# Kernel tuning notes

Measured on AMD Instinct MI355X. Metric: run time of the kernel, lower is better.

The kernel has to match this reference:

```python
import jax, jax.numpy as jnp
import numpy as np

B, D, H = 2048, 1024, 16
DH = D // H            # 64 head dim
R = DH // 2            # 32 random-feature dim (kernel_type has no 'northogonal')
EPS = 1e-3             # keras LayerNormalization default epsilon


def _orthogonal(seed):
    # mirrors random_orthogonal(shape=(1,H,1,DH,R)): QR of flat (H*DH, R) matrix
    rng = np.random.default_rng(seed)
    a = rng.standard_normal((H * DH, R)).astype(np.float32)
    q, r = np.linalg.qr(a)
    q = q * np.sign(np.diag(r))[None, :]
    return jnp.asarray(q.reshape(H, DH, R))


def setup_inputs() -> dict:
    key = jax.random.key(0)
    ks = jax.random.split(key, 8)
    inp = {
        "x": jax.random.normal(ks[0], (B, D), jnp.float32),
        # states start as small positive values so den = phi4(q) . new_z > 0
        "s": jax.random.uniform(ks[1], (B, D * R), jnp.float32),
        "z": jax.random.uniform(ks[2], (B, R * H), jnp.float32),
        "ln1_g": jnp.ones((D,), jnp.float32),
        "ln1_b": jnp.zeros((D,), jnp.float32),
        "ln2_g": jnp.ones((D,), jnp.float32),
        "ln2_b": jnp.zeros((D,), jnp.float32),
        "W_attn": jax.random.normal(ks[3], (D, 3 * D), jnp.float32) * 0.02,
        "b_attn": jnp.zeros((3 * D,), jnp.float32),
        "W_proj": jax.random.normal(ks[4], (D, D), jnp.float32) * 0.02,
        "b_proj": jnp.zeros((D,), jnp.float32),
        "W_fc": jax.random.normal(ks[5], (D, 4 * D), jnp.float32) * 0.02,
        "b_fc": jnp.zeros((4 * D,), jnp.float32),
        "W_mp": jax.random.normal(ks[6], (4 * D, D), jnp.float32) * 0.02,
        "b_mp": jnp.zeros((D,), jnp.float32),
    }
    for i in range(4):
        inp[f"w{i + 1}"] = _orthogonal(100 + i)
    return inp


def _ln(x, g, b):
    m = jnp.mean(x, axis=-1, keepdims=True)
    v = jnp.var(x, axis=-1, keepdims=True)
    return g * (x - m) * jax.lax.rsqrt(v + EPS) + b


def _phi(x, w):
    # x: [B,H,dh], w: [H,dh,R] orthogonal random features; kernel 'sigmoid'
    return jax.nn.sigmoid(jnp.einsum('bhd,hdr->bhr', x, w))


def reference(x, s, z, ln1_g, ln1_b, ln2_g, ln2_b, W_attn, b_attn,
              W_proj, b_proj, W_fc, b_fc, W_mp, b_mp, w1, w2, w3, w4):
    bsz = x.shape[0]
    h1 = _ln(x, ln1_g, ln1_b)
    qkv = h1 @ W_attn + b_attn                      # [B, 3D]
    q, k, v = jnp.split(qkv, 3, axis=1)
    q = q.reshape(bsz, H, DH)
    k = k.reshape(bsz, H, DH)
    v = v.reshape(bsz, H, DH)
    s4 = s.reshape(bsz, H, R, DH)
    z3 = z.reshape(bsz, H, R)
    # kernelized linear-attention state update (outer-product accumulation)
    new_s = s4 + jnp.einsum('bhr,bhd->bhrd', _phi(k, w1), v)   # [B,H,R,DH]
    new_z = z3 + _phi(k, w2)                                   # [B,H,R]
    num = jnp.einsum('bhr,bhrd->bhd', _phi(q, w3), new_s)      # [B,H,DH]
    den = jnp.einsum('bhr,bhr->bh', _phi(q, w4), new_z)[..., None]
    head = (num / den).reshape(bsz, D)
    attention = head @ W_proj + b_proj
    h2 = _ln(attention + x, ln2_g, ln2_b)          # dropout: inference mode
    ffn = jax.nn.gelu(h2 @ W_fc + b_fc, approximate=False) @ W_mp + b_mp
    out = h2 + ffn
    return out, new_s.reshape(bsz, D * R), new_z.reshape(bsz, R * H)
```

## Files before the change

### kernel.cpp

```cpp
#include <hip/hip_runtime.h>
#include <hip/hip_bf16.h>
#include <math.h>


#define Bsz 2048
#define Dm  1024
#define Hh  16
#define DHd 64
#define Rr  32

typedef __bf16 bf16x8 __attribute__((ext_vector_type(8)));
typedef float  f32x4  __attribute__((ext_vector_type(4)));

__device__ __forceinline__ __bf16 f2bf(float x) { return (__bf16)x; }

#define GLOAD_LDS16(g, l) __builtin_amdgcn_global_load_lds(               \
    (const __attribute__((address_space(1))) void*)(g),                   \
    (__attribute__((address_space(3))) void*)(l), 16, 0, 0)

__global__ __launch_bounds__(256) void wtrans_kernel(
    const float* __restrict__ W, __bf16* __restrict__ Wt, int K, int N)
{
  __shared__ float tile[32][33];
  const int tx = threadIdx.x & 31;
  const int ty0 = threadIdx.x >> 5;
  const int bn = blockIdx.x * 32;
  const int bk = blockIdx.y * 32;
#pragma unroll
  for (int j = 0; j < 4; ++j)
    tile[ty0 + j * 8][tx] = W[(size_t)(bk + ty0 + j * 8) * N + bn + tx];
  __syncthreads();
#pragma unroll
  for (int j = 0; j < 4; ++j) {
    const int ny = ty0 + j * 8;
    Wt[(size_t)(bn + ny) * K + bk + tx] = f2bf(tile[tx][ny]);
  }
}

template<bool ADD, typename TA>
__global__ __launch_bounds__(256) void ln_kernel(
    const TA* __restrict__ a, const float* __restrict__ b2,
    const float* __restrict__ g, const float* __restrict__ beta,
    __bf16* __restrict__ outb, float* __restrict__ outf)
{
  const int row = blockIdx.x;
  const int t = threadIdx.x;
  const size_t base = (size_t)row * Dm;
  float vals[4];
#pragma unroll
  for (int i = 0; i < 4; ++i) {
    const int c = t * 4 + i;
    float v = (float)a[base + c];
    if (ADD) v += b2[base + c];
    vals[i] = v;
  }
  float sm = 0.f, sq = 0.f;
#pragma unroll
  for (int i = 0; i < 4; ++i) { sm += vals[i]; sq += vals[i] * vals[i]; }
  for (int off = 32; off > 0; off >>= 1) {
    sm += __shfl_down(sm, off);
    sq += __shfl_down(sq, off);
  }
  __shared__ float smw[4], sqw[4];
  if ((t & 63) == 0) { smw[t >> 6] = sm; sqw[t >> 6] = sq; }
  __syncthreads();
  const float S  = smw[0] + smw[1] + smw[2] + smw[3];
  const float SS = sqw[0] + sqw[1] + sqw[2] + sqw[3];
  const float mean = S * (1.f / Dm);
  const float var  = SS * (1.f / Dm) - mean * mean;
  const float inv  = rsqrtf(var + 1e-3f);
#pragma unroll
  for (int i = 0; i < 4; ++i) {
    const int c = t * 4 + i;
    const float r = g[c] * ((vals[i] - mean) * inv) + beta[c];
    outb[base + c] = f2bf(r);
    if (ADD) outf[base + c] = r;
  }
}

template<int BM, int BN, bool GELU, bool RES, bool OUTF32>
__global__ __launch_bounds__(256) void gemm_kernel(
    const __bf16* __restrict__ A, const __bf16* __restrict__ Bt,
    const float* __restrict__ bias, const float* __restrict__ res,
    void* __restrict__ Cv, int M, int N, int K)
{
  constexpr int FM = BM / 32;
  constexpr int FN = BN / 32;
  __shared__ __align__(16) __bf16 lsA[BM * 32];
  __shared__ __align__(16) __bf16 lsB[BN * 32];
  const int t = threadIdx.x;
  const int wave = t >> 6, lane = t & 63;
  const int quad = lane >> 4, l16 = lane & 15;
  const int wm = wave >> 1, wn = wave & 1;
  const int bm = blockIdx.x * BM, bn = blockIdx.y * BN;

  const int srow = lane >> 2, scol = (lane & 3) * 8;
  const __bf16* Ag  = A  + (size_t)(bm + wave * 16 + srow) * K + scol;
  const __bf16* Bg0 = Bt + (size_t)(bn + wave * (BN / 4) + srow) * K + scol;
  const __bf16* Bg1 = Bt + (size_t)(bn + wave * (BN / 4) + 16 + srow) * K + scol;
  __bf16* lA  = &lsA[wave * 16 * 32];
  __bf16* lB0 = &lsB[wave * (BN / 4) * 32];
  __bf16* lB1 = &lsB[(wave * (BN / 4) + 16) * 32];

  f32x4 acc[FM][FN];
#pragma unroll
  for (int mi = 0; mi < FM; ++mi)
#pragma unroll
    for (int ni = 0; ni < FN; ++ni)
      acc[mi][ni] = (f32x4){0.f, 0.f, 0.f, 0.f};

  for (int kt = 0; kt < K; kt += 32) {
    GLOAD_LDS16(Ag + kt, lA);
    GLOAD_LDS16(Bg0 + kt, lB0);
    if constexpr (BN == 128) GLOAD_LDS16(Bg1 + kt, lB1);
    __syncthreads();
    bf16x8 af[FM], bfr[FN];
#pragma unroll
    for (int mi = 0; mi < FM; ++mi)
      af[mi] = *(const bf16x8*)&lsA[(wm * (BM / 2) + mi * 16 + l16) * 32 + quad * 8];
#pragma unroll
    for (int ni = 0; ni < FN; ++ni)
      bfr[ni] = *(const bf16x8*)&lsB[(wn * (BN / 2) + ni * 16 + l16) * 32 + quad * 8];
#pragma unroll
    for (int mi = 0; mi < FM; ++mi)
#pragma unroll
      for (int ni = 0; ni < FN; ++ni)
        acc[mi][ni] = __builtin_amdgcn_mfma_f32_16x16x32_bf16(
            af[mi], bfr[ni], acc[mi][ni], 0, 0, 0);
    __syncthreads();
  }

#pragma unroll
  for (int mi = 0; mi < FM; ++mi) {
    const int row0 = bm + wm * (BM / 2) + mi * 16 + quad * 4;
#pragma unroll
    for (int ni = 0; ni < FN; ++ni) {
      const int col = bn + wn * (BN / 2) + ni * 16 + l16;
      const float bv = bias[col];
#pragma unroll
      for (int i = 0; i < 4; ++i) {
        const int row = row0 + i;
        float v = acc[mi][ni][i] + bv;
        if (GELU) v = 0.5f * v * (1.0f + erff(v * 0.70710678118654752f));
        if (RES) v += res[(size_t)row * N + col];
        if (OUTF32) ((float*)Cv)[(size_t)row * N + col] = v;
        else        ((__bf16*)Cv)[(size_t)row * N + col] = f2bf(v);
      }
    }
  }
}

__global__ __launch_bounds__(64) void attn_kernel(
    const float* __restrict__ qkv, const float* __restrict__ s,
    const float* __restrict__ z,
    const float* __restrict__ w1, const float* __restrict__ w2,
    const float* __restrict__ w3, const float* __restrict__ w4,
    float* __restrict__ new_s, float* __restrict__ new_z,
    __bf16* __restrict__ head)
{
  const int bh = blockIdx.x;
  const int b = bh >> 4, h = bh & 15;
  const int tid = threadIdx.x;
  __shared__ float ksh[64], qsh[64];
  __shared__ float phish[4][32];
  __shared__ float nzsh[32];

  const float* qrow = qkv + (size_t)b * (3 * Dm);
  const float qv = qrow[h * 64 + tid];
  const float kv = qrow[Dm + h * 64 + tid];
  const float vv = qrow[2 * Dm + h * 64 + tid];
  qsh[tid] = qv; ksh[tid] = kv;
  __syncthreads();

  {
    const int r = tid & 31;
    const float* wm[4] = {w1, w2, w3, w4};
    for (int mm = (tid >> 5); mm < 4; mm += 2) {
      const float* w = wm[mm] + (size_t)h * (DHd * Rr) + r;
      const float* src = (mm < 2) ? ksh : qsh;
      float acc = 0.f;
#pragma unroll 8
      for (int d = 0; d < 64; ++d) acc += src[d] * w[(size_t)d * 32];
      phish[mm][r] = 1.f / (1.f + expf(-acc));
    }
  }
  __syncthreads();

  const size_t zbase = (size_t)b * (Rr * Hh) + h * Rr;
  if (tid < 32) {
    const float nz = z[zbase + tid] + phish[1][tid];
    new_z[zbase + tid] = nz;
    nzsh[tid] = nz;
  }
  __syncthreads();

  float den = 0.f;
#pragma unroll
  for (int r = 0; r < 32; ++r) den += phish[3][r] * nzsh[r];

  const size_t sbase = ((size_t)b * Hh + h) * (Rr * DHd);
  float num = 0.f;
#pragma unroll 4
  for (int r = 0; r < 32; ++r) {
    const float ns = s[sbase + r * 64 + tid] + phish[0][r] * vv;
    new_s[sbase + r * 64 + tid] = ns;
    num += phish[2][r] * ns;
  }
  head[(size_t)b * Dm + h * 64 + tid] = f2bf(num / den);
}

extern "C" void kernel_launch(void* const* d_in, const int* in_sizes, int n_in,
                              void* d_out, int out_size, void* d_ws, size_t ws_size,
                              hipStream_t stream)
{
  const float* x      = (const float*)d_in[0];
  const float* s_in   = (const float*)d_in[1];
  const float* z_in   = (const float*)d_in[2];
  const float* ln1_g  = (const float*)d_in[3];
  const float* ln1_b  = (const float*)d_in[4];
  const float* ln2_g  = (const float*)d_in[5];
  const float* ln2_b  = (const float*)d_in[6];
  const float* W_attn = (const float*)d_in[7];
  const float* b_attn = (const float*)d_in[8];
  const float* W_proj = (const float*)d_in[9];
  const float* b_proj = (const float*)d_in[10];
  const float* W_fc   = (const float*)d_in[11];
  const float* b_fc   = (const float*)d_in[12];
  const float* W_mp   = (const float*)d_in[13];
  const float* b_mp   = (const float*)d_in[14];
  const float* w1     = (const float*)d_in[15];
  const float* w2     = (const float*)d_in[16];
  const float* w3     = (const float*)d_in[17];
  const float* w4     = (const float*)d_in[18];

  float* out0  = (float*)d_out;
  float* out_s = out0 + (size_t)Bsz * Dm;
  float* out_z = out_s + (size_t)Bsz * Dm * Rr;

  char* ws = (char*)d_ws;
  __bf16* h1    = (__bf16*)(ws);
  float*  qkv   = (float*) (ws + ((size_t)4  << 20));
  __bf16* headp = (__bf16*)(ws + ((size_t)28 << 20));
  __bf16* attnb = (__bf16*)(ws + ((size_t)32 << 20));
  __bf16* h2b   = (__bf16*)(ws + ((size_t)36 << 20));
  float*  h2f   = (float*) (ws + ((size_t)40 << 20));
  __bf16* fcb   = (__bf16*)(ws + ((size_t)48 << 20));
  __bf16* Wt_attn = (__bf16*)(ws + ((size_t)48 << 20));
  __bf16* Wt_proj = (__bf16*)(ws + ((size_t)54 << 20));
  __bf16* Wt_fc   = (__bf16*)(ws + ((size_t)4  << 20));
  __bf16* Wt_mp   = (__bf16*)(ws + ((size_t)12 << 20));

  wtrans_kernel<<<dim3((3 * Dm) / 32, Dm / 32), 256, 0, stream>>>(
      W_attn, Wt_attn, Dm, 3 * Dm);
  wtrans_kernel<<<dim3(Dm / 32, Dm / 32), 256, 0, stream>>>(
      W_proj, Wt_proj, Dm, Dm);

  ln_kernel<false, float><<<Bsz, 256, 0, stream>>>(
      x, nullptr, ln1_g, ln1_b, h1, nullptr);
  gemm_kernel<64, 128, false, false, true>
      <<<dim3(Bsz / 64, (3 * Dm) / 128), 256, 0, stream>>>(
      h1, Wt_attn, b_attn, nullptr, qkv, Bsz, 3 * Dm, Dm);
  attn_kernel<<<Bsz * Hh, 64, 0, stream>>>(qkv, s_in, z_in, w1, w2, w3, w4,
                                           out_s, out_z, headp);

  wtrans_kernel<<<dim3((4 * Dm) / 32, Dm / 32), 256, 0, stream>>>(
      W_fc, Wt_fc, Dm, 4 * Dm);
  wtrans_kernel<<<dim3(Dm / 32, (4 * Dm) / 32), 256, 0, stream>>>(
      W_mp, Wt_mp, 4 * Dm, Dm);

  gemm_kernel<64, 64, false, false, false>
      <<<dim3(Bsz / 64, Dm / 64), 256, 0, stream>>>(
      headp, Wt_proj, b_proj, nullptr, attnb, Bsz, Dm, Dm);
  ln_kernel<true, __bf16><<<Bsz, 256, 0, stream>>>(
      attnb, x, ln2_g, ln2_b, h2b, h2f);
  gemm_kernel<64, 128, true, false, false>
      <<<dim3(Bsz / 64, (4 * Dm) / 128), 256, 0, stream>>>(
      h2b, Wt_fc, b_fc, nullptr, fcb, Bsz, 4 * Dm, Dm);
  gemm_kernel<64, 64, false, true, true>
      <<<dim3(Bsz / 64, Dm / 64), 256, 0, stream>>>(
      fcb, Wt_mp, b_mp, h2f, out0, Bsz, Dm, 4 * Dm);
}
```

Before: 701.5 us.

## Generalize GEMM tile loads, use 128x128 tiles, and pack four heads per attention block

The GEMM loader is generalized so any multiple-of-64 tile size works, and the QKV and FC GEMMs switch to 128x128 tiles for more reuse per LDS load. The attention kernel now processes four (batch, head) pairs per 256-thread block, one per wave, and streams the state with float4 loads and stores plus a shuffle reduction for the numerator. This targets the memory-bound state update and per-block launch overhead, at the cost of more registers in the GEMM and fewer GEMM blocks in flight.

```diff
diff --git a/kernel.cpp b/kernel.cpp
--- a/kernel.cpp
+++ b/kernel.cpp
@@ -10,6 +10,7 @@
 #define Rr  32
 
 typedef __bf16 bf16x8 __attribute__((ext_vector_type(8)));
+typedef __bf16 bf16x4 __attribute__((ext_vector_type(4)));
 typedef float  f32x4  __attribute__((ext_vector_type(4)));
 
 __device__ __forceinline__ __bf16 f2bf(float x) { return (__bf16)x; }
@@ -95,12 +96,6 @@
   const int bm = blockIdx.x * BM, bn = blockIdx.y * BN;
 
   const int srow = lane >> 2, scol = (lane & 3) * 8;
-  const __bf16* Ag  = A  + (size_t)(bm + wave * 16 + srow) * K + scol;
-  const __bf16* Bg0 = Bt + (size_t)(bn + wave * (BN / 4) + srow) * K + scol;
-  const __bf16* Bg1 = Bt + (size_t)(bn + wave * (BN / 4) + 16 + srow) * K + scol;
-  __bf16* lA  = &lsA[wave * 16 * 32];
-  __bf16* lB0 = &lsB[wave * (BN / 4) * 32];
-  __bf16* lB1 = &lsB[(wave * (BN / 4) + 16) * 32];
 
   f32x4 acc[FM][FN];
 #pragma unroll
@@ -110,9 +105,14 @@
       acc[mi][ni] = (f32x4){0.f, 0.f, 0.f, 0.f};
 
   for (int kt = 0; kt < K; kt += 32) {
-    GLOAD_LDS16(Ag + kt, lA);
-    GLOAD_LDS16(Bg0 + kt, lB0);
-    if constexpr (BN == 128) GLOAD_LDS16(Bg1 + kt, lB1);
+#pragma unroll
+    for (int i = 0; i < BM / 64; ++i)
+      GLOAD_LDS16(A + (size_t)(bm + i * 64 + wave * 16 + srow) * K + kt + scol,
+                  &lsA[(i * 64 + wave * 16) * 32]);
+#pragma unroll
+    for (int i = 0; i < BN / 64; ++i)
+      GLOAD_LDS16(Bt + (size_t)(bn + i * 64 + wave * 16 + srow) * K + kt + scol,
+                  &lsB[(i * 64 + wave * 16) * 32]);
     __syncthreads();
     bf16x8 af[FM], bfr[FN];
 #pragma unroll
@@ -150,7 +150,7 @@
   }
 }
 
-__global__ __launch_bounds__(64) void attn_kernel(
+__global__ __launch_bounds__(256) void attn_kernel(
     const float* __restrict__ qkv, const float* __restrict__ s,
     const float* __restrict__ z,
     const float* __restrict__ w1, const float* __restrict__ w2,
@@ -158,55 +158,70 @@
     float* __restrict__ new_s, float* __restrict__ new_z,
     __bf16* __restrict__ head)
 {
-  const int bh = blockIdx.x;
+  const int wave = threadIdx.x >> 6, lane = threadIdx.x & 63;
+  const int bh = blockIdx.x * 4 + wave;
   const int b = bh >> 4, h = bh & 15;
-  const int tid = threadIdx.x;
-  __shared__ float ksh[64], qsh[64];
-  __shared__ float phish[4][32];
-  __shared__ float nzsh[32];
-
-  const float* qrow = qkv + (size_t)b * (3 * Dm);
-  const float qv = qrow[h * 64 + tid];
-  const float kv = qrow[Dm + h * 64 + tid];
-  const float vv = qrow[2 * Dm + h * 64 + tid];
-  qsh[tid] = qv; ksh[tid] = kv;
+  __shared__ float ksh[4][64], qsh[4][64], vsh[4][64];
+  __shared__ float phish[4][4][32];
+  __shared__ float nzsh[4][32];
+
+  const float* qrow = qkv + (size_t)b * (3 * Dm) + h * 64 + lane;
+  qsh[wave][lane] = qrow[0];
+  ksh[wave][lane] = qrow[Dm];
+  vsh[wave][lane] = qrow[2 * Dm];
   __syncthreads();
 
   {
-    const int r = tid & 31;
-    const float* wm[4] = {w1, w2, w3, w4};
-    for (int mm = (tid >> 5); mm < 4; mm += 2) {
-      const float* w = wm[mm] + (size_t)h * (DHd * Rr) + r;
-      const float* src = (mm < 2) ? ksh : qsh;
+    const int r = lane & 31;
+    for (int it = 0; it < 2; ++it) {
+      const int mm = (lane >> 5) + it * 2;
+      const float* wp = (mm == 0) ? w1 : (mm == 1) ? w2 : (mm == 2) ? w3 : w4;
+      const float* w = wp + (size_t)h * (DHd * Rr) + r;
+      const float* src = (it == 0) ? ksh[wave] : qsh[wave];
       float acc = 0.f;
 #pragma unroll 8
       for (int d = 0; d < 64; ++d) acc += src[d] * w[(size_t)d * 32];
-      phish[mm][r] = 1.f / (1.f + expf(-acc));
+      phish[wave][mm][r] = 1.f / (1.f + expf(-acc));
     }
   }
   __syncthreads();
 
   const size_t zbase = (size_t)b * (Rr * Hh) + h * Rr;
-  if (tid < 32) {
-    const float nz = z[zbase + tid] + phish[1][tid];
-    new_z[zbase + tid] = nz;
-    nzsh[tid] = nz;
+  if (lane < 32) {
+    const float nz = z[zbase + lane] + phish[wave][1][lane];
+    new_z[zbase + lane] = nz;
+    nzsh[wave][lane] = nz;
   }
   __syncthreads();
 
   float den = 0.f;
 #pragma unroll
-  for (int r = 0; r < 32; ++r) den += phish[3][r] * nzsh[r];
+  for (int r = 0; r < 32; ++r) den += phish[wave][3][r] * nzsh[wave][r];
 
   const size_t sbase = ((size_t)b * Hh + h) * (Rr * DHd);
-  float num = 0.f;
-#pragma unroll 4
-  for (int r = 0; r < 32; ++r) {
-    const float ns = s[sbase + r * 64 + tid] + phish[0][r] * vv;
-    new_s[sbase + r * 64 + tid] = ns;
-    num += phish[2][r] * ns;
-  }
-  head[(size_t)b * Dm + h * 64 + tid] = f2bf(num / den);
+  const int d4 = (lane & 15) * 4, rr = lane >> 4;
+  const f32x4 vv4 = *(const f32x4*)&vsh[wave][d4];
+  f32x4 num4 = {0.f, 0.f, 0.f, 0.f};
+#pragma unroll
+  for (int rb = 0; rb < 8; ++rb) {
+    const int r = rb * 4 + rr;
+    f32x4 sv = *(const f32x4*)(s + sbase + r * 64 + d4);
+    const f32x4 ns = sv + phish[wave][0][r] * vv4;
+    *(f32x4*)(new_s + sbase + r * 64 + d4) = ns;
+    num4 += phish[wave][2][r] * ns;
+  }
+#pragma unroll
+  for (int i = 0; i < 4; ++i) {
+    num4[i] += __shfl_xor(num4[i], 16);
+    num4[i] += __shfl_xor(num4[i], 32);
+  }
+  if (rr == 0) {
+    const float inv = 1.f / den;
+    bf16x4 hv;
+#pragma unroll
+    for (int i = 0; i < 4; ++i) hv[i] = f2bf(num4[i] * inv);
+    *(bf16x4*)(head + (size_t)b * Dm + h * 64 + d4) = hv;
+  }
 }
 
 extern "C" void kernel_launch(void* const* d_in, const int* in_sizes, int n_in,
@@ -257,11 +272,11 @@
 
   ln_kernel<false, float><<<Bsz, 256, 0, stream>>>(
       x, nullptr, ln1_g, ln1_b, h1, nullptr);
-  gemm_kernel<64, 128, false, false, true>
-      <<<dim3(Bsz / 64, (3 * Dm) / 128), 256, 0, stream>>>(
+  gemm_kernel<128, 128, false, false, true>
+      <<<dim3(Bsz / 128, (3 * Dm) / 128), 256, 0, stream>>>(
       h1, Wt_attn, b_attn, nullptr, qkv, Bsz, 3 * Dm, Dm);
-  attn_kernel<<<Bsz * Hh, 64, 0, stream>>>(qkv, s_in, z_in, w1, w2, w3, w4,
-                                           out_s, out_z, headp);
+  attn_kernel<<<Bsz * Hh / 4, 256, 0, stream>>>(qkv, s_in, z_in, w1, w2, w3, w4,
+                                                out_s, out_z, headp);
 
   wtrans_kernel<<<dim3((4 * Dm) / 32, Dm / 32), 256, 0, stream>>>(
       W_fc, Wt_fc, Dm, 4 * Dm);
@@ -273,8 +288,8 @@
       headp, Wt_proj, b_proj, nullptr, attnb, Bsz, Dm, Dm);
   ln_kernel<true, __bf16><<<Bsz, 256, 0, stream>>>(
       attnb, x, ln2_g, ln2_b, h2b, h2f);
-  gemm_kernel<64, 128, true, false, false>
-      <<<dim3(Bsz / 64, (4 * Dm) / 128), 256, 0, stream>>>(
+  gemm_kernel<128, 128, true, false, false>
+      <<<dim3(Bsz / 128, (4 * Dm) / 128), 256, 0, stream>>>(
       h2b, Wt_fc, b_fc, nullptr, fcb, Bsz, 4 * Dm, Dm);
   gemm_kernel<64, 64, false, true, true>
       <<<dim3(Bsz / 64, Dm / 64), 256, 0, stream>>>(
```

After: 685.7 us. 1.02x faster.
